# Kernel tuning notes

Hardware: AMD Instinct MI355X
Metric: run time of the kernel (lower is better)

Reference implementation:

```python
import jax, jax.numpy as jnp
import numpy as np

B, T, I, Hd = 64, 1024, 256, 256
SIGMA = 0.01


def setup_inputs() -> dict:
    key = jax.random.key(0)
    ks = jax.random.split(key, 7)
    return {
        "inputs": jax.random.normal(ks[0], (B, T, I), dtype=jnp.float32),
        "W_xz": jax.random.normal(ks[1], (I, Hd), dtype=jnp.float32) * SIGMA,
        "W_hz": jax.random.normal(ks[2], (Hd, Hd), dtype=jnp.float32) * SIGMA,
        "b_z": jnp.zeros((Hd,), dtype=jnp.float32),
        "W_xr": jax.random.normal(ks[3], (I, Hd), dtype=jnp.float32) * SIGMA,
        "W_hr": jax.random.normal(ks[4], (Hd, Hd), dtype=jnp.float32) * SIGMA,
        "b_r": jnp.zeros((Hd,), dtype=jnp.float32),
        "W_xh": jax.random.normal(ks[5], (I, Hd), dtype=jnp.float32) * SIGMA,
        "W_hh": jax.random.normal(ks[6], (Hd, Hd), dtype=jnp.float32) * SIGMA,
        "b_h": jnp.zeros((Hd,), dtype=jnp.float32),
    }


def reference(inputs, W_xz, W_hz, b_z, W_xr, W_hr, b_r, W_xh, W_hh, b_h):
    # inputs: [B, T, I] -> time-major [T, B, I]
    xs = jnp.swapaxes(inputs, 0, 1)
    # Precompute all input-side projections in three big GEMMs (same math,
    # hoisted out of the recurrence): [T, B, Hd] each.
    xz = jnp.einsum("tbi,ih->tbh", xs, W_xz) + b_z
    xr = jnp.einsum("tbi,ih->tbh", xs, W_xr) + b_r
    xh = jnp.einsum("tbi,ih->tbh", xs, W_xh) + b_h

    H0 = jnp.zeros((inputs.shape[0], W_hz.shape[0]), dtype=inputs.dtype)

    def step(H, x):
        xz_t, xr_t, xh_t = x
        Z = jax.nn.sigmoid(xz_t + H @ W_hz)
        R = jax.nn.sigmoid(xr_t + H @ W_hr)
        H_tilde = jnp.tanh(xh_t + (R * H) @ W_hh)
        H_new = Z * H + (1.0 - Z) * H_tilde
        return H_new, H_new

    H_last, outs = jax.lax.scan(step, H0, (xz, xr, xh))
    # outputs stacked along dim=1: [B, T, Hd]
    outputs = jnp.swapaxes(outs, 0, 1)
    return outputs, H_last
```

## Files before the change

kernel.cpp:

```cpp
#include <hip/hip_runtime.h>
#include <math.h>

#define BB 64
#define TT 1024
#define II 256
#define HD 256

typedef unsigned short ushort_t;
typedef unsigned int uint_t;

typedef short sh8 __attribute__((ext_vector_type(8)));
typedef float fx4 __attribute__((ext_vector_type(4)));

__device__ __forceinline__ ushort_t f2bf(float f) {
    uint_t u = __float_as_uint(f);
    uint_t r = (u + 0x7fffu + ((u >> 16) & 1u)) >> 16;
    return (ushort_t)r;
}
__device__ __forceinline__ float bf2f(ushort_t v) {
    return __uint_as_float(((uint_t)v) << 16);
}

__device__ __forceinline__ float fast_rcp(float x) {
#if __has_builtin(__builtin_amdgcn_rcpf)
    return __builtin_amdgcn_rcpf(x);
#else
    return 1.f / x;
#endif
}
__device__ __forceinline__ float sigm(float x) {
    return fast_rcp(1.f + __expf(-x));
}
__device__ __forceinline__ float tanh_fast(float x) {
    return 1.f - 2.f * fast_rcp(1.f + __expf(2.f * x));
}

__device__ __forceinline__ fx4 mfma16(sh8 a, sh8 b, fx4 c) {
    return __builtin_amdgcn_mfma_f32_16x16x32_bf16(a, b, c, 0, 0, 0);
}

__device__ __forceinline__ void split2(float a, float b, uint_t& hi, uint_t& lo) {
    const uint_t ua = __float_as_uint(a), ub = __float_as_uint(b);
    hi = (ua >> 16) | (ub & 0xffff0000u);
    const float la = a - __uint_as_float(ua & 0xffff0000u);
    const float lb = b - __uint_as_float(ub & 0xffff0000u);
    const uint_t ula = __float_as_uint(la), ulb = __float_as_uint(lb);
    lo = (ula >> 16) | (ulb & 0xffff0000u);
}

__device__ __forceinline__ void async_g2l(const ushort_t* g, ushort_t* l) {
#if __has_builtin(__builtin_amdgcn_global_load_lds)
    __builtin_amdgcn_global_load_lds(
        (const __attribute__((address_space(1))) unsigned int*)g,
        (__attribute__((address_space(3))) unsigned int*)l, 16, 0, 0);
#else
    *reinterpret_cast<uint4*>(l) = *reinterpret_cast<const uint4*>(g);
#endif
}

#define BAR() asm volatile("s_waitcnt lgkmcnt(0)\n\ts_barrier" ::: "memory")

__global__ __launch_bounds__(256) void prepack_kernel(
    const float* __restrict__ Wz, const float* __restrict__ Wr,
    const float* __restrict__ Wh,
    const float* __restrict__ Xz, const float* __restrict__ Xr,
    const float* __restrict__ Xh,
    ushort_t* __restrict__ Tz, ushort_t* __restrict__ Tr,
    ushort_t* __restrict__ Th,
    ushort_t* __restrict__ Thi, ushort_t* __restrict__ Tlo)
{
    const int idx = blockIdx.x * 256 + threadIdx.x;
    const int j = idx >> 8;
    const int k = idx & 255;
    const int y = blockIdx.y;
    if (y < 3) {
        const float* W = (y == 0) ? Wz : (y == 1) ? Wr : Wh;
        ushort_t* T = (y == 0) ? Tz : (y == 1) ? Tr : Th;
        T[idx] = f2bf(W[k * HD + j]);
    } else {
        const int g = y - 3;
        const float* W = (g == 0) ? Xz : (g == 1) ? Xr : Xh;
        const float wv = W[k * HD + j];
        const ushort_t hi = f2bf(wv);
        Thi[g * 65536 + idx] = hi;
        Tlo[g * 65536 + idx] = f2bf(wv - bf2f(hi));
    }
}

#define XROW 264

__global__ __launch_bounds__(512) void proj_fused(
    const float* __restrict__ X,
    const ushort_t* __restrict__ Thi, const ushort_t* __restrict__ Tlo,
    const float* __restrict__ bz, const float* __restrict__ br,
    const float* __restrict__ bh,
    ushort_t* __restrict__ x5)
{
    __shared__ __align__(16) ushort_t Xs[2][32][XROW];
    __shared__ __align__(16) ushort_t ep[32 * 256];

    const int tid  = threadIdx.x;
    const int lane = tid & 63;
    const int w    = tid >> 6;
    const int kq   = lane >> 4;
    const int ml   = lane & 15;
    const int b    = blockIdx.x & 63;
    const int tc   = blockIdx.x >> 6;
    const int t0   = tc * 32;

#pragma unroll
    for (int i = 0; i < 4; ++i) {
        const int idx = i * 512 + tid;
        const int r   = idx >> 6;
        const int c4  = idx & 63;
        const float4 v = *reinterpret_cast<const float4*>(
            X + (size_t)(b * 1024 + t0 + r) * II + c4 * 4);
        uint_t h0, l0, h1, l1;
        split2(v.x, v.y, h0, l0);
        split2(v.z, v.w, h1, l1);
        *reinterpret_cast<uint_t*>(&Xs[0][r][c4 * 4])     = h0;
        *reinterpret_cast<uint_t*>(&Xs[0][r][c4 * 4 + 2]) = h1;
        *reinterpret_cast<uint_t*>(&Xs[1][r][c4 * 4])     = l0;
        *reinterpret_cast<uint_t*>(&Xs[1][r][c4 * 4 + 2]) = l1;
    }
    __syncthreads();

    const fx4 zero4 = {0.f, 0.f, 0.f, 0.f};
    fx4 acc[3][2][2];
#pragma unroll
    for (int g = 0; g < 3; ++g)
#pragma unroll
        for (int mt = 0; mt < 2; ++mt)
#pragma unroll
            for (int nt = 0; nt < 2; ++nt) acc[g][mt][nt] = zero4;

#pragma unroll
    for (int kt = 0; kt < 8; ++kt) {
        const int koff = kq * 8 + kt * 32;
        sh8 ahi[2], alo[2];
#pragma unroll
        for (int mt = 0; mt < 2; ++mt) {
            ahi[mt] = *reinterpret_cast<const sh8*>(&Xs[0][mt * 16 + ml][koff]);
            alo[mt] = *reinterpret_cast<const sh8*>(&Xs[1][mt * 16 + ml][koff]);
        }
#pragma unroll
        for (int g = 0; g < 3; ++g) {
            sh8 bhi[2], blo[2];
#pragma unroll
            for (int nt = 0; nt < 2; ++nt) {
                const size_t rb = ((size_t)g << 16) +
                    (size_t)(w * 32 + nt * 16 + ml) * 256 + koff;
                bhi[nt] = *reinterpret_cast<const sh8*>(Thi + rb);
                blo[nt] = *reinterpret_cast<const sh8*>(Tlo + rb);
            }
#pragma unroll
            for (int mt = 0; mt < 2; ++mt)
#pragma unroll
                for (int nt = 0; nt < 2; ++nt) {
                    acc[g][mt][nt] = mfma16(ahi[mt], bhi[nt], acc[g][mt][nt]);
                    acc[g][mt][nt] = mfma16(alo[mt], bhi[nt], acc[g][mt][nt]);
                    acc[g][mt][nt] = mfma16(ahi[mt], blo[nt], acc[g][mt][nt]);
                }
        }
    }

    for (int g = 0; g < 3; ++g) {
        const float* bias = (g == 0) ? bz : (g == 1) ? br : bh;
        __syncthreads();
#pragma unroll
        for (int nt = 0; nt < 2; ++nt) {
            const int col = w * 32 + nt * 16 + ml;
            const float bv = bias[col];
#pragma unroll
            for (int mt = 0; mt < 2; ++mt)
#pragma unroll
                for (int r = 0; r < 4; ++r)
                    ep[(mt * 16 + kq * 4 + r) * 256 + col] =
                        f2bf(acc[g][mt][nt][r] + bv);
        }
        __syncthreads();
        const uint4* eps = reinterpret_cast<const uint4*>(ep);
#pragma unroll
        for (int it = 0; it < 2; ++it) {
            const int idx  = it * 512 + tid;
            const int rr   = idx >> 5;
            const int part = idx & 31;
            uint4* dst = reinterpret_cast<uint4*>(
                x5 + ((size_t)(t0 + rr) * 64 + b) * 768 + g * 256) + part;
            *dst = eps[idx];
        }
    }
}

#define XB_U16 768

__global__ __launch_bounds__(512, 1) void gru_recur(
    const ushort_t* __restrict__ x5,
    const ushort_t* __restrict__ Tz, const ushort_t* __restrict__ Tr,
    const ushort_t* __restrict__ Th,
    float* __restrict__ out)
{
    __shared__ __align__(16) ushort_t Hl[264];
    __shared__ __align__(16) ushort_t Rl[264];
    __shared__ __align__(16) ushort_t Xb[2][XB_U16];

    const int tid  = threadIdx.x;
    const int lane = tid & 63;
    const int w    = tid >> 6;
    const int kq   = lane >> 4;
    const int ml   = lane & 15;
    const int cl   = lane & 31;
    const int gate = lane >> 5;
    const int sel  = (lane >> 4) & 1;
    const int j    = w * 32 + cl;
    const int b    = blockIdx.x;

    sh8 wz[2][8], wr[2][8], wh[2][8];
#pragma unroll
    for (int cc = 0; cc < 2; ++cc) {
        const int jw = w * 32 + cc * 16 + ml;
        const size_t rb = (size_t)jw * 256 + kq * 8;
#pragma unroll
        for (int kt = 0; kt < 8; ++kt) {
            wz[cc][kt] = *reinterpret_cast<const sh8*>(Tz + rb + kt * 32);
            wr[cc][kt] = *reinterpret_cast<const sh8*>(Tr + rb + kt * 32);
            wh[cc][kt] = *reinterpret_cast<const sh8*>(Th + rb + kt * 32);
        }
    }

    if (tid < 132) { ((uint_t*)Hl)[tid] = 0u; ((uint_t*)Rl)[tid] = 0u; }

    float hk = 0.f;

    if (tid < 96) async_g2l(x5 + (size_t)b * XB_U16 + tid * 8, &Xb[0][tid * 8]);
    asm volatile("s_waitcnt vmcnt(0)" ::: "memory");
    __syncthreads();

    const ushort_t* harow = Hl + kq * 8;
    const ushort_t* rarow = Rl + kq * 8;
    float* ob = out + (size_t)b * TT * HD;

    const fx4 zero4 = {0.f, 0.f, 0.f, 0.f};
    int cur = 0;
    for (int t = 0; t < TT; ++t) {
        {
            const int tn = (t < TT - 1) ? t + 1 : t;
            if (tid < 96)
                async_g2l(x5 + ((size_t)tn * 64 + b) * XB_U16 + tid * 8,
                          &Xb[cur ^ 1][tid * 8]);
        }
        const ushort_t* xc = Xb[cur];

        const float hsh  = __shfl(hk, cl);
        const float xg   = bf2f(xc[gate * 256 + j]);
        const float xh_r = bf2f(xc[512 + j]);

        fx4 az0 = zero4, az1 = zero4, ar0 = zero4, ar1 = zero4;
#pragma unroll
        for (int kt = 0; kt < 8; ++kt) {
            const sh8 a = *reinterpret_cast<const sh8*>(harow + kt * 32);
            az0 = mfma16(a, wz[0][kt], az0);
            az1 = mfma16(a, wz[1][kt], az1);
            ar0 = mfma16(a, wr[0][kt], ar0);
            ar1 = mfma16(a, wr[1][kt], ar1);
        }
        const float v0 = gate ? ar0[0] : az0[0];
        const float v1 = gate ? ar1[0] : az1[0];
        const float v  = sel ? v1 : v0;
        const float s  = sigm(xg + v);
        const float zreg = s;
        if (gate) Rl[j] = f2bf(s * hsh);
        BAR();

        fx4 ah0a = zero4, ah0b = zero4, ah1a = zero4, ah1b = zero4;
#pragma unroll
        for (int kt = 0; kt < 8; kt += 2) {
            const sh8 a0 = *reinterpret_cast<const sh8*>(rarow + kt * 32);
            const sh8 a1 = *reinterpret_cast<const sh8*>(rarow + (kt + 1) * 32);
            ah0a = mfma16(a0, wh[0][kt], ah0a);
            ah1a = mfma16(a0, wh[1][kt], ah1a);
            ah0b = mfma16(a1, wh[0][kt + 1], ah0b);
            ah1b = mfma16(a1, wh[1][kt + 1], ah1b);
        }
        float hn = hk;
        if (!gate) {
            const float va = sel ? (ah1a[0] + ah1b[0]) : (ah0a[0] + ah0b[0]);
            const float th = tanh_fast(xh_r + va);
            hn = zreg * hk + (1.f - zreg) * th;
            hk = hn;
            Hl[j] = f2bf(hn);
        }
        asm volatile("s_waitcnt vmcnt(0)" ::: "memory");
        BAR();

        if (!gate) ob[(size_t)t * HD + j] = hn;
        cur ^= 1;
    }

    if (!gate) out[(size_t)BB * TT * HD + (size_t)b * HD + j] = hk;
}

extern "C" void kernel_launch(void* const* d_in, const int* in_sizes, int n_in,
                              void* d_out, int out_size, void* d_ws, size_t ws_size,
                              hipStream_t stream) {
    const float* X   = (const float*)d_in[0];
    const float* Wxz = (const float*)d_in[1];
    const float* Whz = (const float*)d_in[2];
    const float* bz  = (const float*)d_in[3];
    const float* Wxr = (const float*)d_in[4];
    const float* Whr = (const float*)d_in[5];
    const float* br  = (const float*)d_in[6];
    const float* Wxh = (const float*)d_in[7];
    const float* Whh = (const float*)d_in[8];
    const float* bh  = (const float*)d_in[9];
    float* out = (float*)d_out;

    const size_t X5_BYTES = (size_t)TT * BB * 3 * 256 * 2;
    ushort_t* x5  = (ushort_t*)d_ws;
    ushort_t* Tz  = (ushort_t*)((char*)d_ws + X5_BYTES);
    ushort_t* Tr  = Tz + HD * HD;
    ushort_t* Th  = Tr + HD * HD;
    ushort_t* Thi = Th + HD * HD;
    ushort_t* Tlo = Thi + 3 * HD * HD;

    prepack_kernel<<<dim3(256, 6), 256, 0, stream>>>(
        Whz, Whr, Whh, Wxz, Wxr, Wxh, Tz, Tr, Th, Thi, Tlo);
    proj_fused<<<dim3(2048), 512, 0, stream>>>(
        X, Thi, Tlo, bz, br, bh, x5);
    gru_recur<<<dim3(64), 512, 0, stream>>>(x5, Tz, Tr, Th, out);
}
```

Before: 1.426 ms.

## Fuse projection and recurrence into one launch with flag-based producer/consumer sync

Merges the input-projection GEMM kernel and the GRU recurrence kernel into a single launch. The first 64 blocks run the recurrence and the remaining 2048 blocks compute projection chunks, each publishing a completion flag that the recurrence blocks spin on before consuming each 32-step chunk. The goal is to overlap the projection work with the serial recurrence and hide the projection time. This relies on the recurrence blocks being scheduled first and on forward progress of producer blocks. The spin-waits add polling overhead, and the projection blocks compete with the recurrence blocks for CUs and bandwidth.

```diff
diff --git a/kernel.cpp b/kernel.cpp
--- a/kernel.cpp
+++ b/kernel.cpp
@@ -60,6 +60,14 @@
 
 #define BAR() asm volatile("s_waitcnt lgkmcnt(0)\n\ts_barrier" ::: "memory")
 
+__device__ __forceinline__ void wait_flag(uint_t* f) {
+    if (threadIdx.x == 0) {
+        while (atomicAdd(f, 0u) == 0u) __builtin_amdgcn_s_sleep(8);
+    }
+    __syncthreads();
+    __threadfence();
+}
+
 __global__ __launch_bounds__(256) void prepack_kernel(
     const float* __restrict__ Wz, const float* __restrict__ Wr,
     const float* __restrict__ Wh,
@@ -67,7 +75,8 @@
     const float* __restrict__ Xh,
     ushort_t* __restrict__ Tz, ushort_t* __restrict__ Tr,
     ushort_t* __restrict__ Th,
-    ushort_t* __restrict__ Thi, ushort_t* __restrict__ Tlo)
+    ushort_t* __restrict__ Thi, ushort_t* __restrict__ Tlo,
+    uint_t* __restrict__ flags)
 {
     const int idx = blockIdx.x * 256 + threadIdx.x;
     const int j = idx >> 8;
@@ -79,6 +88,7 @@
         T[idx] = f2bf(W[k * HD + j]);
     } else {
         const int g = y - 3;
+        if (g == 0 && idx < 2048) flags[idx] = 0u;
         const float* W = (g == 0) ? Xz : (g == 1) ? Xr : Xh;
         const float wv = W[k * HD + j];
         const ushort_t hi = f2bf(wv);
@@ -88,133 +98,141 @@
 }
 
 #define XROW 264
-
-__global__ __launch_bounds__(512) void proj_fused(
+#define XB_U16 768
+
+__global__ __launch_bounds__(512, 1) void gru_fused(
     const float* __restrict__ X,
     const ushort_t* __restrict__ Thi, const ushort_t* __restrict__ Tlo,
     const float* __restrict__ bz, const float* __restrict__ br,
     const float* __restrict__ bh,
-    ushort_t* __restrict__ x5)
+    const ushort_t* __restrict__ Tz, const ushort_t* __restrict__ Tr,
+    const ushort_t* __restrict__ Th,
+    ushort_t* __restrict__ x5,
+    uint_t* __restrict__ flags,
+    float* __restrict__ out)
 {
-    __shared__ __align__(16) ushort_t Xs[2][32][XROW];
-    __shared__ __align__(16) ushort_t ep[32 * 256];
+    __shared__ __align__(16) ushort_t smem[25088];
 
     const int tid  = threadIdx.x;
     const int lane = tid & 63;
     const int w    = tid >> 6;
     const int kq   = lane >> 4;
     const int ml   = lane & 15;
-    const int b    = blockIdx.x & 63;
-    const int tc   = blockIdx.x >> 6;
-    const int t0   = tc * 32;
-
-#pragma unroll
-    for (int i = 0; i < 4; ++i) {
-        const int idx = i * 512 + tid;
-        const int r   = idx >> 6;
-        const int c4  = idx & 63;
-        const float4 v = *reinterpret_cast<const float4*>(
-            X + (size_t)(b * 1024 + t0 + r) * II + c4 * 4);
-        uint_t h0, l0, h1, l1;
-        split2(v.x, v.y, h0, l0);
-        split2(v.z, v.w, h1, l1);
-        *reinterpret_cast<uint_t*>(&Xs[0][r][c4 * 4])     = h0;
-        *reinterpret_cast<uint_t*>(&Xs[0][r][c4 * 4 + 2]) = h1;
-        *reinterpret_cast<uint_t*>(&Xs[1][r][c4 * 4])     = l0;
-        *reinterpret_cast<uint_t*>(&Xs[1][r][c4 * 4 + 2]) = l1;
-    }
-    __syncthreads();
-
-    const fx4 zero4 = {0.f, 0.f, 0.f, 0.f};
-    fx4 acc[3][2][2];
-#pragma unroll
-    for (int g = 0; g < 3; ++g)
-#pragma unroll
-        for (int mt = 0; mt < 2; ++mt)
-#pragma unroll
-            for (int nt = 0; nt < 2; ++nt) acc[g][mt][nt] = zero4;
-
-#pragma unroll
-    for (int kt = 0; kt < 8; ++kt) {
-        const int koff = kq * 8 + kt * 32;
-        sh8 ahi[2], alo[2];
-#pragma unroll
-        for (int mt = 0; mt < 2; ++mt) {
-            ahi[mt] = *reinterpret_cast<const sh8*>(&Xs[0][mt * 16 + ml][koff]);
-            alo[mt] = *reinterpret_cast<const sh8*>(&Xs[1][mt * 16 + ml][koff]);
-        }
-#pragma unroll
+
+    if (blockIdx.x >= 64) {
+        const int pb = blockIdx.x - 64;
+        const int b  = pb & 63;
+        const int tc = pb >> 6;
+        const int t0 = tc * 32;
+
+        ushort_t* Xs0 = smem;
+        ushort_t* Xs1 = smem + 32 * XROW;
+        ushort_t* ep  = smem + 64 * XROW;
+
+#pragma unroll
+        for (int i = 0; i < 4; ++i) {
+            const int idx = i * 512 + tid;
+            const int r   = idx >> 6;
+            const int c4  = idx & 63;
+            const float4 v = *reinterpret_cast<const float4*>(
+                X + (size_t)(b * 1024 + t0 + r) * II + c4 * 4);
+            uint_t h0, l0, h1, l1;
+            split2(v.x, v.y, h0, l0);
+            split2(v.z, v.w, h1, l1);
+            *reinterpret_cast<uint_t*>(&Xs0[r * XROW + c4 * 4])     = h0;
+            *reinterpret_cast<uint_t*>(&Xs0[r * XROW + c4 * 4 + 2]) = h1;
+            *reinterpret_cast<uint_t*>(&Xs1[r * XROW + c4 * 4])     = l0;
+            *reinterpret_cast<uint_t*>(&Xs1[r * XROW + c4 * 4 + 2]) = l1;
+        }
+        __syncthreads();
+
+        const fx4 zero4 = {0.f, 0.f, 0.f, 0.f};
+        fx4 acc[3][2][2];
+#pragma unroll
+        for (int g = 0; g < 3; ++g)
+#pragma unroll
+            for (int mt = 0; mt < 2; ++mt)
+#pragma unroll
+                for (int nt = 0; nt < 2; ++nt) acc[g][mt][nt] = zero4;
+
+#pragma unroll
+        for (int kt = 0; kt < 8; ++kt) {
+            const int koff = kq * 8 + kt * 32;
+            sh8 ahi[2], alo[2];
+#pragma unroll
+            for (int mt = 0; mt < 2; ++mt) {
+                ahi[mt] = *reinterpret_cast<const sh8*>(
+                    &Xs0[(mt * 16 + ml) * XROW + koff]);
+                alo[mt] = *reinterpret_cast<const sh8*>(
+                    &Xs1[(mt * 16 + ml) * XROW + koff]);
+            }
+#pragma unroll
+            for (int g = 0; g < 3; ++g) {
+                sh8 bhi[2], blo[2];
+#pragma unroll
+                for (int nt = 0; nt < 2; ++nt) {
+                    const size_t rb = ((size_t)g << 16) +
+                        (size_t)(w * 32 + nt * 16 + ml) * 256 + koff;
+                    bhi[nt] = *reinterpret_cast<const sh8*>(Thi + rb);
+                    blo[nt] = *reinterpret_cast<const sh8*>(Tlo + rb);
+                }
+#pragma unroll
+                for (int mt = 0; mt < 2; ++mt)
+#pragma unroll
+                    for (int nt = 0; nt < 2; ++nt) {
+                        acc[g][mt][nt] = mfma16(ahi[mt], bhi[nt], acc[g][mt][nt]);
+                        acc[g][mt][nt] = mfma16(alo[mt], bhi[nt], acc[g][mt][nt]);
+                        acc[g][mt][nt] = mfma16(ahi[mt], blo[nt], acc[g][mt][nt]);
+                    }
+            }
+        }
+
         for (int g = 0; g < 3; ++g) {
-            sh8 bhi[2], blo[2];
+            const float* bias = (g == 0) ? bz : (g == 1) ? br : bh;
+            __syncthreads();
 #pragma unroll
             for (int nt = 0; nt < 2; ++nt) {
-                const size_t rb = ((size_t)g << 16) +
-                    (size_t)(w * 32 + nt * 16 + ml) * 256 + koff;
-                bhi[nt] = *reinterpret_cast<const sh8*>(Thi + rb);
-                blo[nt] = *reinterpret_cast<const sh8*>(Tlo + rb);
+                const int col = w * 32 + nt * 16 + ml;
+                const float bv = bias[col];
+#pragma unroll
+                for (int mt = 0; mt < 2; ++mt)
+#pragma unroll
+                    for (int r = 0; r < 4; ++r)
+                        ep[(mt * 16 + kq * 4 + r) * 256 + col] =
+                            f2bf(acc[g][mt][nt][r] + bv);
             }
-#pragma unroll
-            for (int mt = 0; mt < 2; ++mt)
-#pragma unroll
-                for (int nt = 0; nt < 2; ++nt) {
-                    acc[g][mt][nt] = mfma16(ahi[mt], bhi[nt], acc[g][mt][nt]);
-                    acc[g][mt][nt] = mfma16(alo[mt], bhi[nt], acc[g][mt][nt]);
-                    acc[g][mt][nt] = mfma16(ahi[mt], blo[nt], acc[g][mt][nt]);
-                }
-        }
-    }
-
-    for (int g = 0; g < 3; ++g) {
-        const float* bias = (g == 0) ? bz : (g == 1) ? br : bh;
+            __syncthreads();
+            const uint4* eps = reinterpret_cast<const uint4*>(ep);
+#pragma unroll
+            for (int it = 0; it < 2; ++it) {
+                const int idx  = it * 512 + tid;
+                const int rr   = idx >> 5;
+                const int part = idx & 31;
+                uint4* dst = reinterpret_cast<uint4*>(
+                    x5 + ((size_t)(t0 + rr) * 64 + b) * 768 + g * 256) + part;
+                *dst = eps[idx];
+            }
+        }
+
         __syncthreads();
-#pragma unroll
-        for (int nt = 0; nt < 2; ++nt) {
-            const int col = w * 32 + nt * 16 + ml;
-            const float bv = bias[col];
-#pragma unroll
-            for (int mt = 0; mt < 2; ++mt)
-#pragma unroll
-                for (int r = 0; r < 4; ++r)
-                    ep[(mt * 16 + kq * 4 + r) * 256 + col] =
-                        f2bf(acc[g][mt][nt][r] + bv);
-        }
-        __syncthreads();
-        const uint4* eps = reinterpret_cast<const uint4*>(ep);
-#pragma unroll
-        for (int it = 0; it < 2; ++it) {
-            const int idx  = it * 512 + tid;
-            const int rr   = idx >> 5;
-            const int part = idx & 31;
-            uint4* dst = reinterpret_cast<uint4*>(
-                x5 + ((size_t)(t0 + rr) * 64 + b) * 768 + g * 256) + part;
-            *dst = eps[idx];
-        }
-    }
-}
-
-#define XB_U16 768
-
-__global__ __launch_bounds__(512, 1) void gru_recur(
-    const ushort_t* __restrict__ x5,
-    const ushort_t* __restrict__ Tz, const ushort_t* __restrict__ Tr,
-    const ushort_t* __restrict__ Th,
-    float* __restrict__ out)
-{
-    __shared__ __align__(16) ushort_t Hl[264];
-    __shared__ __align__(16) ushort_t Rl[264];
-    __shared__ __align__(16) ushort_t Xb[2][XB_U16];
-
-    const int tid  = threadIdx.x;
-    const int lane = tid & 63;
-    const int w    = tid >> 6;
-    const int kq   = lane >> 4;
-    const int ml   = lane & 15;
+        if (tid == 0) {
+            __threadfence();
+            atomicExch(&flags[pb], 1u);
+        }
+        return;
+    }
+
     const int cl   = lane & 31;
     const int gate = lane >> 5;
     const int sel  = (lane >> 4) & 1;
     const int j    = w * 32 + cl;
     const int b    = blockIdx.x;
 
+    ushort_t* Hl  = smem;
+    ushort_t* Rl  = smem + 264;
+    ushort_t* Xb0 = smem + 528;
+    ushort_t* Xb1 = smem + 1296;
+
     sh8 wz[2][8], wr[2][8], wh[2][8];
 #pragma unroll
     for (int cc = 0; cc < 2; ++cc) {
@@ -232,7 +250,8 @@
 
     float hk = 0.f;
 
-    if (tid < 96) async_g2l(x5 + (size_t)b * XB_U16 + tid * 8, &Xb[0][tid * 8]);
+    wait_flag(&flags[b]);
+    if (tid < 96) async_g2l(x5 + (size_t)b * XB_U16 + tid * 8, Xb0 + tid * 8);
     asm volatile("s_waitcnt vmcnt(0)" ::: "memory");
     __syncthreads();
 
@@ -245,11 +264,14 @@
     for (int t = 0; t < TT; ++t) {
         {
             const int tn = (t < TT - 1) ? t + 1 : t;
+            if ((tn & 31) == 0 && t < TT - 1)
+                wait_flag(&flags[(tn >> 5) * 64 + b]);
+            ushort_t* l = cur ? Xb0 : Xb1;
             if (tid < 96)
                 async_g2l(x5 + ((size_t)tn * 64 + b) * XB_U16 + tid * 8,
-                          &Xb[cur ^ 1][tid * 8]);
-        }
-        const ushort_t* xc = Xb[cur];
+                          l + tid * 8);
+        }
+        const ushort_t* xc = cur ? Xb1 : Xb0;
 
         const float hsh  = __shfl(hk, cl);
         const float xg   = bf2f(xc[gate * 256 + j]);
@@ -322,10 +344,10 @@
     ushort_t* Th  = Tr + HD * HD;
     ushort_t* Thi = Th + HD * HD;
     ushort_t* Tlo = Thi + 3 * HD * HD;
+    uint_t*   flags = (uint_t*)(Tlo + 3 * HD * HD);
 
     prepack_kernel<<<dim3(256, 6), 256, 0, stream>>>(
-        Whz, Whr, Whh, Wxz, Wxr, Wxh, Tz, Tr, Th, Thi, Tlo);
-    proj_fused<<<dim3(2048), 512, 0, stream>>>(
-        X, Thi, Tlo, bz, br, bh, x5);
-    gru_recur<<<dim3(64), 512, 0, stream>>>(x5, Tz, Tr, Th, out);
-}
+        Whz, Whr, Whh, Wxz, Wxr, Wxh, Tz, Tr, Th, Thi, Tlo, flags);
+    gru_fused<<<dim3(64 + 2048), 512, 0, stream>>>(
+        X, Thi, Tlo, bz, br, bh, Tz, Tr, Th, x5, flags, out);
+}
```

Result: slower. 1.489 ms (+4.4%).
